# Kernel tuning notes

Measured on AMD Instinct MI355X. Metric: run time of the kernel, lower is better.

## Reference

```python
import jax, jax.numpy as jnp
import numpy as np

B, L, D, N = 4, 8192, 128, 32


def setup_inputs() -> dict:
    key = jax.random.key(0)
    ks = jax.random.split(key, 12)
    s = 0.05  # small init scale for stability of exp/cumsum
    return {
        "x": jax.random.normal(ks[0], (B, L, D), jnp.float32),
        "h_t_minus_1": jax.random.normal(ks[1], (B, L, D), jnp.float32),
        "A_log": jax.random.normal(ks[2], (D, N), jnp.float32),
        "D_param": jnp.ones((D,), jnp.float32),
        "W_x": jax.random.normal(ks[3], (D, 2 * N + D), jnp.float32) * s,
        "W_dt": jax.random.normal(ks[4], (D, D), jnp.float32) * s,
        "b_dt": jnp.zeros((D,), jnp.float32),
        "conv_w": jax.random.normal(ks[5], (3, D, D), jnp.float32) * s,  # (width, in, out)
        "conv_b": jnp.zeros((D,), jnp.float32),
        "W_f": jax.random.normal(ks[6], (D, D), jnp.float32) * s,
        "b_f": jnp.zeros((D,), jnp.float32),
    }


def reference(x, h_t_minus_1, A_log, D_param, W_x, W_dt, b_dt, conv_w, conv_b, W_f, b_f):
    d, n = A_log.shape
    A = -jnp.exp(A_log)  # (d, n)
    x_dbl = x @ W_x  # (b, l, d + 2n)
    delta, Bm, Cm = jnp.split(x_dbl, [d, d + n], axis=-1)
    delta = jax.nn.softplus(delta @ W_dt + b_dt)  # (b, l, d)

    # selective scan
    dA = jnp.einsum('bld,dn->bldn', delta, A)
    dB_u = jnp.einsum('bld,bld,bln->bldn', delta, h_t_minus_1, Bm)
    dA_cumsum = jnp.exp(jnp.cumsum(dA, axis=1) - dA)  # exclusive cumsum
    h_t = jnp.einsum('bldn,bln->bld', dB_u * dA_cumsum, Cm)
    h_t = h_t + h_t * D_param

    ssm_output = jax.nn.relu(h_t @ W_f + b_f)
    # causal Conv1D, kernel=3: left-pad by 2
    conv = jax.lax.conv_general_dilated(
        ssm_output, conv_w, window_strides=(1,), padding=[(2, 0)],
        dimension_numbers=('NWC', 'WIO', 'NWC')) + conv_b
    causal_output = jax.nn.relu(conv)
    fused_output = ssm_output * causal_output
    return (fused_output, h_t)
```

## Files before the change

kernel.cpp:

```cpp
#include <hip/hip_runtime.h>
#include <math.h>

typedef unsigned short u16;
typedef __attribute__((ext_vector_type(8))) short short8v;
typedef __attribute__((ext_vector_type(4))) float f32x4;

constexpr int B_  = 4;
constexpr int L_  = 8192;
constexpr int D_  = 128;
constexpr int N_  = 32;
constexpr int BL  = B_ * L_;
constexpr int CH  = 16;
constexpr int NC  = L_ / CH;
constexpr int SCH = 32;
constexpr int SNC = L_ / SCH;

__device__ inline unsigned bfr(float x) {
    unsigned u = __float_as_uint(x);
    return (u + 0x7fffu + ((u >> 16) & 1u)) >> 16;
}
__device__ inline unsigned pkbf(float a, float b) { return bfr(a) | (bfr(b) << 16); }
__device__ inline float b2f(u16 h) { return __uint_as_float(((unsigned)h) << 16); }

__global__ __launch_bounds__(512) void prep(
    const float* __restrict__ Wx, const float* __restrict__ Wdt,
    const float* __restrict__ Wf, const float* __restrict__ Wconv,
    const float* __restrict__ A_log,
    u16* __restrict__ Wt0, u16* __restrict__ Wt2, u16* __restrict__ Wtc,
    float* __restrict__ negAT, float* __restrict__ amax)
{
    const int y = blockIdx.y;
    const int tid = threadIdx.x;
    constexpr float L2E = 1.4426950408889634f;
    if (y == 0) {
        if (blockIdx.x >= 32) return;
        __shared__ float wd[128 * 128];
        #pragma unroll
        for (int j = 0; j < 8; ++j) {
            const int g = tid + j * 512;
            *reinterpret_cast<float4*>(&wd[g * 4]) =
                *reinterpret_cast<const float4*>(&Wdt[(size_t)g * 4]);
        }
        __syncthreads();
        const int k = blockIdx.x * 4 + (tid >> 7);
        const int d = tid & 127;
        float s = 0.f;
        #pragma unroll 8
        for (int j = 0; j < 128; ++j)
            s = fmaf(Wx[(size_t)k * 192 + j], wd[j * 128 + d], s);
        Wt0[d * 128 + k] = (u16)bfr(s);
        return;
    }
    const int t = blockIdx.x * 512 + tid;
    if (y == 1) {
        if (t >= 64 * 128) return;
        const int n = t >> 7, k = t & 127;
        Wt0[(128 + n) * 128 + k] = (u16)bfr(Wx[(size_t)k * 192 + 128 + n]);
    } else if (y == 2) {
        if (t >= 128 * 128) return;
        const int n = t >> 7, k = t & 127;
        Wt2[n * 128 + k] = (u16)bfr(Wf[(size_t)k * 128 + n]);
    } else if (y <= 5) {
        if (t >= 128 * 128) return;
        const int w = y - 3;
        const int n = t >> 7, k = t & 127;
        Wtc[((size_t)w * 128 + n) * 128 + k] = (u16)bfr(Wconv[((size_t)w * 128 + k) * 128 + n]);
    } else if (y == 6) {
        if (t >= 128 * 32) return;
        const int d = t >> 5, n = t & 31;
        negAT[n * 128 + d] = -expf(A_log[d * 32 + n]) * L2E;
    } else {
        if (t >= 128) return;
        float m = -1e30f;
        for (int n = 0; n < 32; ++n)
            m = fmaxf(m, -expf(A_log[t * 32 + n]) * L2E);
        amax[t] = m;
    }
}

__global__ __launch_bounds__(256) void gemm1(
    const float* __restrict__ x, const u16* __restrict__ Wt0,
    const float* __restrict__ b_dt,
    float* __restrict__ delta, float* __restrict__ bc,
    float* __restrict__ part)
{
    __shared__ __align__(16) u16 Blds[192 * 128];

    const int tid = threadIdx.x;
    const int r0 = blockIdx.x * 64;

    #pragma unroll
    for (int j = 0; j < 12; ++j) {
        const int g = tid + j * 256;
        const int n = g >> 4, k8 = (g & 15) * 8;
        const uint4 p = *reinterpret_cast<const uint4*>(&Wt0[(size_t)n * 128 + k8]);
        *reinterpret_cast<uint4*>(&Blds[n * 128 + (k8 ^ ((n & 7) << 3))]) = p;
    }

    const int w = tid >> 6, lane = tid & 63;
    const int lr = lane & 15, kg = lane >> 4;
    const int arow = r0 + w * 16 + lr;

    float4 av[4][2];
    #pragma unroll
    for (int ks = 0; ks < 4; ++ks) {
        const float* src = &x[(size_t)arow * 128 + ks * 32 + kg * 8];
        av[ks][0] = *reinterpret_cast<const float4*>(src);
        av[ks][1] = *reinterpret_cast<const float4*>(src + 4);
    }
    __syncthreads();

    f32x4 acc[12] = {};
    #pragma unroll
    for (int ks = 0; ks < 4; ++ks) {
        uint4 ap;
        ap.x = pkbf(av[ks][0].x, av[ks][0].y);
        ap.y = pkbf(av[ks][0].z, av[ks][0].w);
        ap.z = pkbf(av[ks][1].x, av[ks][1].y);
        ap.w = pkbf(av[ks][1].z, av[ks][1].w);
        const short8v af = *reinterpret_cast<const short8v*>(&ap);
        const int kb = ks * 32 + kg * 8;
        #pragma unroll
        for (int nf = 0; nf < 12; ++nf) {
            const int n = nf * 16 + lr;
            const short8v bf = *reinterpret_cast<const short8v*>(
                &Blds[n * 128 + (kb ^ ((n & 7) << 3))]);
            acc[nf] = __builtin_amdgcn_mfma_f32_16x16x32_bf16(af, bf, acc[nf], 0, 0, 0);
        }
    }

    const int orow = r0 + w * 16;
    const int bb = orow >> 13;
    const int chk = (orow & (L_ - 1)) >> 4;
    #pragma unroll
    for (int nf = 0; nf < 8; ++nf) {
        const int col = nf * 16 + lr;
        const float bbv = b_dt[col];
        float v[4];
        #pragma unroll
        for (int q = 0; q < 4; ++q) {
            const float t = acc[nf][q] + bbv;
            v[q] = fmaxf(t, 0.f) + log1pf(expf(-fabsf(t)));
        }
        const float g4 = v[0] + v[1] + v[2] + v[3];
        const float g0 = __shfl(g4, lr, 64);
        const float g1 = __shfl(g4, lr + 16, 64);
        const float g2 = __shfl(g4, lr + 32, 64);
        const float g3 = __shfl(g4, lr + 48, 64);
        const size_t rb = (size_t)(orow + kg * 4) * 128 + col;
        delta[rb + 0 * 128] = v[0];
        delta[rb + 1 * 128] = v[1];
        delta[rb + 2 * 128] = v[2];
        delta[rb + 3 * 128] = v[3];
        if (kg == 0)
            part[((size_t)bb * 128 + col) * NC + chk] = g0 + g1 + g2 + g3;
    }
    #pragma unroll
    for (int h2 = 0; h2 < 2; ++h2)
        #pragma unroll
        for (int q = 0; q < 4; ++q)
            bc[(size_t)(orow + kg * 4 + q) * 32 + h2 * 16 + lr] =
                acc[8 + h2][q] * acc[10 + h2][q];
}

__global__ __launch_bounds__(512) void scan_main(
    const float* __restrict__ delta, const float* __restrict__ hprev,
    const float* __restrict__ bc, const float* __restrict__ negAT,
    const float* __restrict__ amax, const float* __restrict__ Dp,
    const float* __restrict__ part,
    float* __restrict__ h_out, u16* __restrict__ hb)
{
    __shared__ float delta_s[SCH * 128];
    __shared__ float at_s[32 * 128];
    __shared__ float bc_s[SCH * 32];
    __shared__ float P_lds[128 * 2];

    const int cb = blockIdx.x, b = blockIdx.y;
    const int tid = threadIdx.x;
    const size_t rowbase = (size_t)b * L_ + (size_t)cb * SCH;

    #pragma unroll
    for (int j = 0; j < 2; ++j) {
        const int g = tid + j * 512;
        reinterpret_cast<float4*>(delta_s)[g] =
            reinterpret_cast<const float4*>(&delta[rowbase * 128])[g];
    }
    #pragma unroll
    for (int j = 0; j < 2; ++j) {
        const int g = tid + j * 512;
        reinterpret_cast<float4*>(at_s)[g] =
            reinterpret_cast<const float4*>(negAT)[g];
    }
    if (tid < 256)
        reinterpret_cast<float4*>(bc_s)[tid] =
            reinterpret_cast<const float4*>(&bc[rowbase * 32])[tid];

    {
        const int dq = tid >> 2, j = tid & 3;
        const size_t pb = ((size_t)b * 128 + dq) * NC;
        const int Cend = cb * 2;
        float e0 = 0.f, e1 = 0.f;
        int c = j;
        for (; c + 4 < Cend; c += 8) {
            e0 += part[pb + c];
            e1 += part[pb + c + 4];
        }
        for (; c < Cend; c += 4) e0 += part[pb + c];
        float e = e0 + e1;
        e += __shfl_xor(e, 1, 64);
        e += __shfl_xor(e, 2, 64);
        if (j == 0) {
            const float extra = part[pb + Cend];
            P_lds[dq * 2]     = e;
            P_lds[dq * 2 + 1] = e + extra;
        }
    }

    const int d = tid & 127, r0 = tid >> 7;
    const float dp1 = 1.f + Dp[d];
    const float am = amax[d];
    __syncthreads();

    const float part0 = P_lds[d * 2];
    const float part1 = P_lds[d * 2 + 1];

    float sv[8];
    {
        float s = part0;
        #pragma unroll
        for (int i = 0; i < 16; ++i) {
            if ((i & 3) == r0) sv[i >> 2] = s;
            s += delta_s[i * 128 + d];
        }
        s = part1;
        #pragma unroll
        for (int i = 16; i < 32; ++i) {
            if ((i & 3) == r0) sv[i >> 2] = s;
            s += delta_s[i * 128 + d];
        }
    }

    #pragma unroll 1
    for (int r = 0; r < 8; ++r) {
        const int row = r * 4 + r0;
        const size_t rb = (rowbase + row) * 128 + d;
        const float S = sv[r];
        float h = 0.f;
        if (__any(S * am >= -80.f)) {
            const float dv = delta_s[row * 128 + d];
            const float hv = hprev[rb];
            float p0 = 0.f, p1 = 0.f, p2 = 0.f, p3 = 0.f;
            #pragma unroll
            for (int n4 = 0; n4 < 8; ++n4) {
                const float4 b4 = *reinterpret_cast<const float4*>(&bc_s[row * 32 + n4 * 4]);
                p0 = fmaf(b4.x, exp2f(S * at_s[(n4 * 4 + 0) * 128 + d]), p0);
                p1 = fmaf(b4.y, exp2f(S * at_s[(n4 * 4 + 1) * 128 + d]), p1);
                p2 = fmaf(b4.z, exp2f(S * at_s[(n4 * 4 + 2) * 128 + d]), p2);
                p3 = fmaf(b4.w, exp2f(S * at_s[(n4 * 4 + 3) * 128 + d]), p3);
            }
            h = dv * hv * ((p0 + p1) + (p2 + p3)) * dp1;
        }
        h_out[rb] = h;
        hb[rb] = (u16)bfr(h);
    }
}

__global__ __launch_bounds__(512) void conv_fuse2(
    const u16* __restrict__ hb, const u16* __restrict__ Wt2,
    const float* __restrict__ b_f, const u16* __restrict__ Wtc,
    const float* __restrict__ cbias, float* __restrict__ fused)
{
    __shared__ __align__(16) u16 hb_s[80 * 128];
    __shared__ __align__(16) u16 ssm_s[80 * 128];

    const int tid = threadIdx.x;
    const int bb = blockIdx.y;
    const int r0 = blockIdx.x * 64;
    const u16* hbB = hb + (size_t)bb * L_ * 128;

    #pragma unroll
    for (int j = 0; j < 3; ++j) {
        const int g = tid + j * 512;
        if (g < 80 * 16) {
            const int s = g >> 4, k8 = (g & 15) * 8;
            const int gr = r0 - 2 + s;
            uint4 p = make_uint4(0, 0, 0, 0);
            if (gr >= 0 && gr < L_)
                p = *reinterpret_cast<const uint4*>(&hbB[(size_t)gr * 128 + k8]);
            *reinterpret_cast<uint4*>(&hb_s[s * 128 + (k8 ^ ((s & 7) << 3))]) = p;
        }
    }
    __syncthreads();

    const int w = tid >> 6, lane = tid & 63;
    const int lr = lane & 15, kg = lane >> 4;

    #pragma unroll
    for (int ui = 0; ui < 5; ++ui) {
        const int u = w * 5 + ui;
        const int sm = u >> 3, nf = u & 7;
        const int col = nf * 16 + lr;
        f32x4 a = {};
        #pragma unroll
        for (int ks = 0; ks < 4; ++ks) {
            const int kb = ks * 32 + kg * 8;
            const int sr = sm * 16 + lr;
            const short8v af = *reinterpret_cast<const short8v*>(
                &hb_s[sr * 128 + (kb ^ ((sr & 7) << 3))]);
            const short8v bf = *reinterpret_cast<const short8v*>(
                &Wt2[(size_t)col * 128 + kb]);
            a = __builtin_amdgcn_mfma_f32_16x16x32_bf16(af, bf, a, 0, 0, 0);
        }
        const float bbv = b_f[col];
        #pragma unroll
        for (int q = 0; q < 4; ++q) {
            const int s2 = sm * 16 + kg * 4 + q;
            float vv = fmaxf(a[q] + bbv, 0.f);
            if (r0 - 2 + s2 < 0) vv = 0.f;
            ssm_s[s2 * 128 + (col ^ ((s2 & 7) << 3))] = (u16)bfr(vv);
        }
    }
    __syncthreads();

    const int wm = w >> 2, wn = w & 3;
    f32x4 acc[2][2] = {};
    #pragma unroll
    for (int ks = 0; ks < 4; ++ks) {
        const int k8 = ks * 32 + kg * 8;
        short8v af[2][3];
        #pragma unroll
        for (int m = 0; m < 2; ++m)
            #pragma unroll
            for (int t = 0; t < 3; ++t) {
                const int ri = wm * 32 + m * 16 + lr + t;
                af[m][t] = *reinterpret_cast<const short8v*>(
                    &ssm_s[ri * 128 + (k8 ^ ((ri & 7) << 3))]);
            }
        #pragma unroll
        for (int nf = 0; nf < 2; ++nf) {
            const int col = wn * 32 + nf * 16 + lr;
            #pragma unroll
            for (int t = 0; t < 3; ++t) {
                const short8v bfg = *reinterpret_cast<const short8v*>(
                    &Wtc[((size_t)t * 128 + col) * 128 + k8]);
                acc[0][nf] = __builtin_amdgcn_mfma_f32_16x16x32_bf16(af[0][t], bfg, acc[0][nf], 0, 0, 0);
                acc[1][nf] = __builtin_amdgcn_mfma_f32_16x16x32_bf16(af[1][t], bfg, acc[1][nf], 0, 0, 0);
            }
        }
    }
    #pragma unroll
    for (int nf = 0; nf < 2; ++nf) {
        const int col = wn * 32 + nf * 16 + lr;
        const float cb2 = cbias[col];
        #pragma unroll
        for (int m = 0; m < 2; ++m)
            #pragma unroll
            for (int q = 0; q < 4; ++q) {
                const int ro = wm * 32 + m * 16 + kg * 4 + q;
                const int ri = ro + 2;
                const u16 sh = ssm_s[ri * 128 + (col ^ ((ri & 7) << 3))];
                const float cv = fmaxf(acc[m][nf][q] + cb2, 0.f);
                fused[((size_t)bb * L_ + r0 + ro) * 128 + col] = b2f(sh) * cv;
            }
    }
}

extern "C" void kernel_launch(void* const* d_in, const int* in_sizes, int n_in,
                              void* d_out, int out_size, void* d_ws, size_t ws_size,
                              hipStream_t stream)
{
    const float* x      = (const float*)d_in[0];
    const float* hprev  = (const float*)d_in[1];
    const float* A_log  = (const float*)d_in[2];
    const float* Dp     = (const float*)d_in[3];
    const float* W_x    = (const float*)d_in[4];
    const float* W_dt   = (const float*)d_in[5];
    const float* b_dt   = (const float*)d_in[6];
    const float* conv_w = (const float*)d_in[7];
    const float* conv_b = (const float*)d_in[8];
    const float* W_f    = (const float*)d_in[9];
    const float* b_f    = (const float*)d_in[10];

    float* out   = (float*)d_out;
    float* h_out = out + (size_t)BL * D_;

    char* ws = (char*)d_ws;
    float* delta = (float*)ws;                  ws += (size_t)BL * 128 * 4;
    float* bcb   = (float*)ws;                  ws += (size_t)BL * 32 * 4;
    float* part  = (float*)ws;                  ws += (size_t)B_ * 128 * NC * 4;
    float* negAT = (float*)ws;                  ws += (size_t)N_ * 128 * 4;
    float* amaxb = (float*)ws;                  ws += (size_t)128 * 4;
    u16*   Wt0   = (u16*)ws;                    ws += (size_t)192 * 128 * 2;
    u16*   Wt2   = (u16*)ws;                    ws += (size_t)128 * 128 * 2;
    u16*   Wtc   = (u16*)ws;                    ws += (size_t)3 * 128 * 128 * 2;
    u16*   hb    = (u16*)ws;

    prep<<<dim3(64, 8), dim3(512), 0, stream>>>(
        W_x, W_dt, W_f, conv_w, A_log, Wt0, Wt2, Wtc, negAT, amaxb);
    gemm1<<<dim3(BL / 64), dim3(256), 0, stream>>>(
        x, Wt0, b_dt, delta, bcb, part);
    scan_main<<<dim3(SNC, B_), dim3(512), 0, stream>>>(
        delta, hprev, bcb, negAT, amaxb, Dp, part, h_out, hb);
    conv_fuse2<<<dim3(L_ / 64, B_), dim3(512), 0, stream>>>(
        hb, Wt2, b_f, Wtc, conv_b, out);
}
```

Before: 183.3 us.

## Precompute chunk prefix sums in a separate kernel and skip fully-underflowed scan blocks

Adds a scan_prefix kernel that computes an exclusive prefix over the per-chunk delta partial sums, stored transposed so each scan block reads its starting offset directly. Previously every scan block re-summed all preceding partials, so the cost grew with its position in the sequence. scan_main now also checks whether exp(cumsum*A) has underflowed for every channel in its chunk (exponent below -80). If so, it writes zeros to h and its bf16 copy and returns early, avoiding the loads and the scan. The change adds one kernel launch and a workspace buffer. The skip relies on the decay having underflowed, which is numerically valid but data-dependent.

```diff
diff --git a/kernel.cpp b/kernel.cpp
--- a/kernel.cpp
+++ b/kernel.cpp
@@ -163,21 +163,68 @@
                 acc[8 + h2][q] * acc[10 + h2][q];
 }
 
-__global__ __launch_bounds__(512) void scan_main(
+__global__ __launch_bounds__(512) void scan_prefix(
+    const float* __restrict__ part, float* __restrict__ part2)
+{
+    const int b = blockIdx.x, d = blockIdx.y;
+    const int c = threadIdx.x, w = c >> 6, lane = c & 63;
+    const size_t base = ((size_t)b * 128 + d) * NC;
+    const float v = part[base + c];
+    float s = v;
+    #pragma unroll
+    for (int off = 1; off < 64; off <<= 1) {
+        const float t = __shfl_up(s, off, 64);
+        if (lane >= off) s += t;
+    }
+    __shared__ float wsum[8];
+    if (lane == 63) wsum[w] = s;
+    __syncthreads();
+    float add = 0.f;
+    #pragma unroll
+    for (int i = 0; i < 8; ++i)
+        if (i < w) add += wsum[i];
+    part2[((size_t)b * NC + c) * 128 + d] = s + add - v;
+}
+
+__global__ __launch_bounds__(512, 4) void scan_main(
     const float* __restrict__ delta, const float* __restrict__ hprev,
     const float* __restrict__ bc, const float* __restrict__ negAT,
     const float* __restrict__ amax, const float* __restrict__ Dp,
-    const float* __restrict__ part,
+    const float* __restrict__ part2,
     float* __restrict__ h_out, u16* __restrict__ hb)
 {
     __shared__ float delta_s[SCH * 128];
     __shared__ float at_s[32 * 128];
     __shared__ float bc_s[SCH * 32];
-    __shared__ float P_lds[128 * 2];
+    __shared__ int   wflag[8];
 
     const int cb = blockIdx.x, b = blockIdx.y;
     const int tid = threadIdx.x;
     const size_t rowbase = (size_t)b * L_ + (size_t)cb * SCH;
+    const int d = tid & 127, r0 = tid >> 7;
+
+    const float am = amax[d];
+    const size_t p2b = ((size_t)b * NC + (size_t)cb * 2) * 128 + d;
+    const float part0 = part2[p2b];
+    const float part1 = part2[p2b + 128];
+
+    const bool need = (part0 * am >= -80.f);
+    const unsigned long long mask = __ballot(need);
+    if ((tid & 63) == 0) wflag[tid >> 6] = (mask != 0ull);
+    __syncthreads();
+    const int anyneed = wflag[0] | wflag[1] | wflag[2] | wflag[3] |
+                        wflag[4] | wflag[5] | wflag[6] | wflag[7];
+
+    if (!anyneed) {
+        float4 z4 = make_float4(0.f, 0.f, 0.f, 0.f);
+        float4* ho = reinterpret_cast<float4*>(&h_out[rowbase * 128]);
+        #pragma unroll
+        for (int j = 0; j < 2; ++j)
+            ho[tid + j * 512] = z4;
+        uint4 zi = make_uint4(0, 0, 0, 0);
+        reinterpret_cast<uint4*>(&hb[rowbase * 128])[tid] = zi;
+        return;
+    }
 
     #pragma unroll
     for (int j = 0; j < 2; ++j) {
@@ -195,34 +242,8 @@
         reinterpret_cast<float4*>(bc_s)[tid] =
             reinterpret_cast<const float4*>(&bc[rowbase * 32])[tid];
 
-    {
-        const int dq = tid >> 2, j = tid & 3;
-        const size_t pb = ((size_t)b * 128 + dq) * NC;
-        const int Cend = cb * 2;
-        float e0 = 0.f, e1 = 0.f;
-        int c = j;
-        for (; c + 4 < Cend; c += 8) {
-            e0 += part[pb + c];
-            e1 += part[pb + c + 4];
-        }
-        for (; c < Cend; c += 4) e0 += part[pb + c];
-        float e = e0 + e1;
-        e += __shfl_xor(e, 1, 64);
-        e += __shfl_xor(e, 2, 64);
-        if (j == 0) {
-            const float extra = part[pb + Cend];
-            P_lds[dq * 2]     = e;
-            P_lds[dq * 2 + 1] = e + extra;
-        }
-    }
-
-    const int d = tid & 127, r0 = tid >> 7;
     const float dp1 = 1.f + Dp[d];
-    const float am = amax[d];
-    __syncthreads();
-
-    const float part0 = P_lds[d * 2];
-    const float part1 = P_lds[d * 2 + 1];
+    __syncthreads();
 
     float sv[8];
     {
@@ -388,6 +409,7 @@
     float* delta = (float*)ws;                  ws += (size_t)BL * 128 * 4;
     float* bcb   = (float*)ws;                  ws += (size_t)BL * 32 * 4;
     float* part  = (float*)ws;                  ws += (size_t)B_ * 128 * NC * 4;
+    float* part2 = (float*)ws;                  ws += (size_t)B_ * NC * 128 * 4;
     float* negAT = (float*)ws;                  ws += (size_t)N_ * 128 * 4;
     float* amaxb = (float*)ws;                  ws += (size_t)128 * 4;
     u16*   Wt0   = (u16*)ws;                    ws += (size_t)192 * 128 * 2;
@@ -399,8 +421,9 @@
         W_x, W_dt, W_f, conv_w, A_log, Wt0, Wt2, Wtc, negAT, amaxb);
     gemm1<<<dim3(BL / 64), dim3(256), 0, stream>>>(
         x, Wt0, b_dt, delta, bcb, part);
+    scan_prefix<<<dim3(B_, D_), dim3(512), 0, stream>>>(part, part2);
     scan_main<<<dim3(SNC, B_), dim3(512), 0, stream>>>(
-        delta, hprev, bcb, negAT, amaxb, Dp, part, h_out, hb);
+        delta, hprev, bcb, negAT, amaxb, Dp, part2, h_out, hb);
     conv_fuse2<<<dim3(L_ / 64, B_), dim3(512), 0, stream>>>(
         hb, Wt2, b_f, Wtc, conv_b, out);
 }
```

New measurement: 174.4 us. 4.8% less time.
